# Optimization experiments

Measured on AMD Instinct MI355X. Metric: run time of the kernel, lower is better.

Reference implementation:

```python
import jax, jax.numpy as jnp
import numpy as np

N = 1024          # total nodes (includes BATCH virtual roots, processed first)
BATCH = 8         # number of trees / images
IN_DIM = 2048     # inputs_dim
EMBED = 200       # embed_dim ('start' token at row 0)
HID = 1024        # hidden_dim
NUM_CLASSES = 151 # len(classes), class 0 = background (never committed)
X_DIM = IN_DIM + EMBED


def setup_inputs() -> dict:
    key = jax.random.key(0)
    ks = jax.random.split(key, 8)
    # topologically-ordered tree: node i's parent is some j < i; first BATCH nodes are roots
    rng = np.random.RandomState(0)
    parent = np.full(N, -1, dtype=np.int64)
    for i in range(BATCH, N):
        parent[i] = rng.randint(0, i)
    sx = 1.0 / np.sqrt(X_DIM)
    sh = 1.0 / np.sqrt(HID)
    return dict(
        features=jax.random.normal(ks[0], (N, IN_DIM), jnp.float32),
        parent_idx=jnp.asarray(parent),
        batch_size=BATCH,
        W_px=jax.random.normal(ks[1], (X_DIM, HID), jnp.float32) * sx,
        b_px=jnp.zeros((HID,), jnp.float32),
        W_iofux=jax.random.normal(ks[2], (X_DIM, 5 * HID), jnp.float32) * sx,
        b_iofux=jnp.zeros((5 * HID,), jnp.float32),
        W_iofuh=jax.random.normal(ks[3], (HID, 5 * HID), jnp.float32) * sh,
        b_iofuh=jnp.zeros((5 * HID,), jnp.float32),
        W_out=jax.random.normal(ks[4], (HID, NUM_CLASSES), jnp.float32) * sh,
        b_out=jnp.zeros((NUM_CLASSES,), jnp.float32),
        embed_table=jax.random.normal(ks[5], (NUM_CLASSES + 1, EMBED), jnp.float32),
    )


def reference(features, parent_idx, batch_size, W_px, b_px, W_iofux, b_iofux,
              W_iofuh, b_iofuh, W_out, b_out, embed_table):
    n = features.shape[0]
    hid = W_iofuh.shape[0]

    def step(carry, i):
        h_all, c_all, commit_all = carry
        p = parent_idx[i]
        root = p < 0
        ps = jnp.maximum(p, 0)
        gate = jnp.where(root, 0.0, 1.0)
        ph = h_all[ps] * gate          # parent hidden (zeros at root)
        pc = c_all[ps] * gate          # parent cell   (zeros at root)
        # parent's committed label embedding; row 0 = 'start' token for roots
        pe = embed_table[jnp.where(root, 0, commit_all[ps])]
        x = jnp.concatenate([features[i], pe])          # [X_DIM]
        proj_x = x @ W_px + b_px                        # highway projection
        g = x @ W_iofux + b_iofux + ph @ W_iofuh + b_iofuh  # [5*HID]
        ig, og, fg, ug, rg = jnp.split(g, 5)
        ig = jax.nn.sigmoid(ig)
        og = jax.nn.sigmoid(og)
        fg = jax.nn.sigmoid(fg)
        rg = jax.nn.sigmoid(rg)
        ug = jnp.tanh(ug)
        c = ig * ug + fg * pc
        h = og * jnp.tanh(c)
        h_final = rg * h + (1.0 - rg) * proj_x          # highway output
        dist = h_final @ W_out + b_out                  # class logits
        # greedy commitment, background (class 0) excluded
        commit = (jnp.argmax(dist[1:]) + 1).astype(jnp.int32)
        carry = (h_all.at[i].set(h_final),
                 c_all.at[i].set(c),
                 commit_all.at[i].set(commit))
        return carry, dist

    init = (jnp.zeros((n, hid), features.dtype),
            jnp.zeros((n, hid), features.dtype),
            jnp.zeros((n,), jnp.int32))
    (h_all, c_all, commit_all), dists = jax.lax.scan(step, init, jnp.arange(n))
    # order puts the batch_size virtual roots last; they are then dropped
    out_dists = dists[batch_size:]
    out_commitments = jnp.concatenate(
        [commit_all[batch_size:], jnp.zeros((batch_size,), jnp.int32)])
    return out_dists, out_commitments
```

## Files before the change

### kernel.cpp

```cpp
#include <hip/hip_runtime.h>
#include <math.h>


#define NBLK 512
#define NTHR 512
#define OUT_COMMIT_OFF (1016 * 151)

typedef short bf16x8 __attribute__((ext_vector_type(8)));
typedef float f32x16 __attribute__((ext_vector_type(16)));

__device__ __align__(16) short g_Wih_hi[160 * 128 * 32 * 8 + 512];
__device__ __align__(16) short g_Wih_lo[160 * 128 * 32 * 8 + 512];
__device__ __align__(16) short g_Wpre_hi[192 * 256 * 32 * 8 + 512];
__device__ __align__(16) short g_Wpre_lo[192 * 256 * 32 * 8 + 512];
__device__ __align__(16) short g_fpk_hi[32 * 256 * 32 * 8 + 512];
__device__ __align__(16) short g_fpk_lo[32 * 256 * 32 * 8 + 512];
__device__ __align__(16) unsigned g_Apk_hi[128 * 128 * 32 * 4 + 256];
__device__ __align__(16) unsigned g_Apk_lo[128 * 128 * 32 * 4 + 256];
__device__ __align__(16) unsigned g_Spk_hi[128 * 128 * 32 * 4 + 256];
__device__ __align__(16) unsigned g_Spk_lo[128 * 128 * 32 * 4 + 256];
__device__ __align__(16) short g_Wout_hi[5 * 128 * 32 * 8 + 512];
__device__ __align__(16) short g_Wout_lo[5 * 128 * 32 * 8 + 512];

__device__ __align__(16) float g_c[1024 * 1024];
__device__ __align__(16) float g_pre[1024 * 6144];
__device__ __align__(16) float g_gate[1120 * 5120];
__device__ __align__(16) float g_embG[152 * 6144];
__device__ __align__(16) float g_embpad[162 * 224];
__device__ __align__(16) float g_zero[128];
__device__ __align__(16) float g_pamax_v[128 * 32 * 5 + 64];
__device__ __align__(16) int   g_pamax_i[128 * 32 * 5 + 64];
__device__ int g_lvl_start[1025];
__device__ int g_tile_off[1025];
__device__ int g_order[1024];
__device__ int g_prow[1024];
__device__ int g_cstart[1025];
__device__ int g_clist[1024];
__device__ int g_numlvl;
__device__ unsigned g_barcnt[512];

__device__ __forceinline__ unsigned short bf16_rn(float x) {
  union { float f; unsigned u; } v; v.f = x;
  unsigned r = v.u + 0x7fffu + ((v.u >> 16) & 1u);
  return (unsigned short)(r >> 16);
}
__device__ __forceinline__ float bf16_tof(unsigned short h) {
  union { float f; unsigned u; } v; v.u = ((unsigned)h) << 16; return v.f;
}
__device__ __forceinline__ void split2(float x, unsigned short& hi, unsigned short& lo) {
  hi = bf16_rn(x);
  lo = bf16_rn(x - bf16_tof(hi));
}
__device__ __forceinline__ f32x16 mfma3(bf16x8 ah, bf16x8 al, bf16x8 bh, bf16x8 bl, f32x16 c) {
  c = __builtin_amdgcn_mfma_f32_32x32x16_bf16(ah, bh, c, 0, 0, 0);
  c = __builtin_amdgcn_mfma_f32_32x32x16_bf16(ah, bl, c, 0, 0, 0);
  c = __builtin_amdgcn_mfma_f32_32x32x16_bf16(al, bh, c, 0, 0, 0);
  return c;
}

#define AST_F(p, v)  __hip_atomic_store((p), (v), __ATOMIC_RELAXED, __HIP_MEMORY_SCOPE_AGENT)
#define AST_U(p, v)  __hip_atomic_store((p), (v), __ATOMIC_RELAXED, __HIP_MEMORY_SCOPE_AGENT)

#define LD8(p, o) (*(const bf16x8*)((p) + (o)))

template<int NS>
__device__ __forceinline__ f32x16 gemm1x(const short* __restrict__ pah,
                                         const short* __restrict__ pal,
                                         const short* __restrict__ pbh,
                                         const short* __restrict__ pbl) {
  f32x16 acc = {};
  bf16x8 ahe = LD8(pah, 0),   ale = LD8(pal, 0);
  bf16x8 bhe = LD8(pbh, 0),   ble = LD8(pbl, 0);
  bf16x8 aho = LD8(pah, 512), alo = LD8(pal, 512);
  bf16x8 bho = LD8(pbh, 512), blo = LD8(pbl, 512);
  for (int g = 0; g + 1 < NS / 2; ++g) {
    const size_t o = (size_t)(2 * g + 2) * 512;
    acc = mfma3(ahe, ale, bhe, ble, acc);
    ahe = LD8(pah, o); ale = LD8(pal, o); bhe = LD8(pbh, o); ble = LD8(pbl, o);
    acc = mfma3(aho, alo, bho, blo, acc);
    aho = LD8(pah, o + 512); alo = LD8(pal, o + 512);
    bho = LD8(pbh, o + 512); blo = LD8(pbl, o + 512);
  }
  acc = mfma3(ahe, ale, bhe, ble, acc);
  acc = mfma3(aho, alo, bho, blo, acc);
  return acc;
}

template<int NS>
__device__ __forceinline__ void gemm2x(const short* __restrict__ pa0h, const short* __restrict__ pa0l,
                                       const short* __restrict__ pa1h, const short* __restrict__ pa1l,
                                       const short* __restrict__ pbh,  const short* __restrict__ pbl,
                                       f32x16& acc0, f32x16& acc1) {
  bf16x8 a0he = LD8(pa0h, 0),   a0le = LD8(pa0l, 0);
  bf16x8 a1he = LD8(pa1h, 0),   a1le = LD8(pa1l, 0);
  bf16x8 bhe  = LD8(pbh, 0),    ble  = LD8(pbl, 0);
  bf16x8 a0ho = LD8(pa0h, 512), a0lo = LD8(pa0l, 512);
  bf16x8 a1ho = LD8(pa1h, 512), a1lo = LD8(pa1l, 512);
  bf16x8 bho  = LD8(pbh, 512),  blo  = LD8(pbl, 512);
  for (int g = 0; g + 1 < NS / 2; ++g) {
    const size_t o = (size_t)(2 * g + 2) * 512;
    acc0 = mfma3(a0he, a0le, bhe, ble, acc0);
    acc1 = mfma3(a1he, a1le, bhe, ble, acc1);
    a0he = LD8(pa0h, o); a0le = LD8(pa0l, o);
    a1he = LD8(pa1h, o); a1le = LD8(pa1l, o);
    bhe = LD8(pbh, o);   ble = LD8(pbl, o);
    acc0 = mfma3(a0ho, a0lo, bho, blo, acc0);
    acc1 = mfma3(a1ho, a1lo, bho, blo, acc1);
    a0ho = LD8(pa0h, o + 512); a0lo = LD8(pa0l, o + 512);
    a1ho = LD8(pa1h, o + 512); a1lo = LD8(pa1l, o + 512);
    bho = LD8(pbh, o + 512);   blo = LD8(pbl, o + 512);
  }
  acc0 = mfma3(a0he, a0le, bhe, ble, acc0);
  acc1 = mfma3(a1he, a1le, bhe, ble, acc1);
  acc0 = mfma3(a0ho, a0lo, bho, blo, acc0);
  acc1 = mfma3(a1ho, a1lo, bho, blo, acc1);
}

__device__ __forceinline__ void gload_lds16(const float* g, float* s) {
  __builtin_amdgcn_global_load_lds(
      (const __attribute__((address_space(1))) void*)g,
      (__attribute__((address_space(3))) void*)s, 16, 0, 0);
}

__device__ __forceinline__ void gbar(unsigned int* gen) {
  __syncthreads();
  if (threadIdx.x == 0) {
    ++(*gen);
    __hip_atomic_fetch_add(&g_barcnt[((unsigned)blockIdx.x & 15) << 5], 1u,
                           __ATOMIC_RELAXED, __HIP_MEMORY_SCOPE_AGENT);
    const unsigned int target = (unsigned int)NBLK * (*gen);
    for (;;) {
      unsigned int s = 0;
      #pragma unroll
      for (int i = 0; i < 16; ++i)
        s += __hip_atomic_load(&g_barcnt[i << 5], __ATOMIC_RELAXED, __HIP_MEMORY_SCOPE_AGENT);
      if (s >= target) break;
      __builtin_amdgcn_s_sleep(8);
    }
  }
  __syncthreads();
}

__device__ __forceinline__ int pamax_combine(int prow) {
  float bv = -3.4e38f; int bi = 1;
  #pragma unroll
  for (int nt = 0; nt < 5; ++nt) {
    const float v = g_pamax_v[prow * 5 + nt];
    const int ii = g_pamax_i[prow * 5 + nt];
    if (v > bv) { bv = v; bi = ii; }
  }
  return bi;
}

__global__ void prep_kernel(const int* __restrict__ parent,
                            const float* __restrict__ emb,
                            float* __restrict__ out) {
  __shared__ int lvl[1024];
  __shared__ int cnt[1024];
  __shared__ int c2[1024];
  __shared__ int changed;
  const int i = threadIdx.x;
  const int p = parent[i];
  lvl[i] = (p < 0) ? 0 : -1;
  for (;;) {
    if (i == 0) changed = 0;
    __syncthreads();
    if (lvl[i] < 0 && lvl[p] >= 0) { lvl[i] = lvl[p] + 1; changed = 1; }
    __syncthreads();
    const int ch = changed;
    __syncthreads();
    if (ch == 0) break;
  }
  cnt[i] = 0;
  __syncthreads();
  atomicAdd(&cnt[lvl[i]], 1);
  __syncthreads();
  if (i == 0) {
    int acc = 0, nl = 0, ta = 0;
    for (int l2 = 0; l2 < 1024; ++l2) {
      g_lvl_start[l2] = acc;
      g_tile_off[l2] = ta;
      if (cnt[l2] > 0) nl = l2 + 1;
      acc += cnt[l2];
      ta += (cnt[l2] + 31) >> 5;
    }
    g_lvl_start[1024] = acc;
    g_tile_off[1024] = ta;
    g_numlvl = nl;
  }
  __syncthreads();
  cnt[i] = 0;
  __syncthreads();
  {
    const int ni = atomicAdd(&cnt[lvl[i]], 1);
    g_order[g_lvl_start[lvl[i]] + ni] = i;
    g_prow[i] = ((g_tile_off[lvl[i]] + (ni >> 5)) << 5) | (ni & 31);
  }
  __syncthreads();
  cnt[i] = 0;
  __syncthreads();
  if (p >= 0) atomicAdd(&cnt[p], 1);
  __syncthreads();
  if (i == 0) {
    int a2 = 0;
    for (int n2 = 0; n2 < 1024; ++n2) { g_cstart[n2] = a2; a2 += cnt[n2]; }
    g_cstart[1024] = a2;
  }
  __syncthreads();
  c2[i] = 0;
  __syncthreads();
  if (p >= 0) {
    const int q = g_cstart[p] + atomicAdd(&c2[p], 1);
    g_clist[q] = i;
  }
  for (int j = i; j < 162 * 224; j += 1024) {
    const int r = j / 224, cc = j - r * 224;
    g_embpad[j] = (r < 152 && cc < 200) ? emb[r * 200 + cc] : 0.0f;
  }
  __syncthreads();
  {
    const int n0 = g_tile_off[1] * 16384;
    for (int e = i; e < n0; e += 1024) { g_Apk_hi[e] = 0u; g_Apk_lo[e] = 0u; }
  }
  if (i < 512) g_barcnt[i] = 0u;
  if (i < 128) g_zero[i] = 0.0f;
  if (i < 8) out[OUT_COMMIT_OFF + 1016 + i] = 0.0f;
}

#define U_WIH  (160 * 128 * 32)
#define U_WPRE (192 * 256 * 32)
#define U_FEAT (32 * 256 * 32)
#define U_WOUT (5 * 128 * 32)
__global__ void pack_all(const float* __restrict__ Wpx, const float* __restrict__ Wix,
                         const float* __restrict__ Wih, const float* __restrict__ feat,
                         const float* __restrict__ Wout) {
  const int tot = U_WIH + U_WPRE + U_FEAT + U_WOUT;
  for (int u = blockIdx.x * blockDim.x + threadIdx.x; u < tot; u += gridDim.x * blockDim.x) {
    if (u < U_WIH) {
      const int j = u & 31, kb = (u >> 5) & 127, nt = u >> 12;
      const int n = nt * 32 + j;
      #pragma unroll
      for (int kk = 0; kk < 8; ++kk) {
        unsigned short h, l;
        split2(Wih[(size_t)(kb * 8 + kk) * 5120 + n], h, l);
        g_Wih_hi[(size_t)u * 8 + kk] = (short)h;
        g_Wih_lo[(size_t)u * 8 + kk] = (short)l;
      }
    } else if (u < U_WIH + U_WPRE) {
      const int u2 = u - U_WIH;
      const int j = u2 & 31, kb = (u2 >> 5) & 255, nt = u2 >> 13;
      const int n = nt * 32 + j;
      #pragma unroll
      for (int kk = 0; kk < 8; ++kk) {
        const int k = kb * 8 + kk;
        const float v = (n < 1024) ? Wpx[(size_t)k * 1024 + n]
                                   : Wix[(size_t)k * 5120 + (n - 1024)];
        unsigned short h, l; split2(v, h, l);
        g_Wpre_hi[(size_t)u2 * 8 + kk] = (short)h;
        g_Wpre_lo[(size_t)u2 * 8 + kk] = (short)l;
      }
    } else if (u < U_WIH + U_WPRE + U_FEAT) {
      const int u3 = u - U_WIH - U_WPRE;
      const int j = u3 & 31, kb = (u3 >> 5) & 255, mt = u3 >> 13;
      const int m = mt * 32 + j;
      #pragma unroll
      for (int kk = 0; kk < 8; ++kk) {
        unsigned short h, l;
        split2(feat[(size_t)m * 2048 + kb * 8 + kk], h, l);
        g_fpk_hi[(size_t)u3 * 8 + kk] = (short)h;
        g_fpk_lo[(size_t)u3 * 8 + kk] = (short)l;
      }
    } else {
      const int u4 = u - U_WIH - U_WPRE - U_FEAT;
      const int j = u4 & 31, kb = (u4 >> 5) & 127, nt = u4 >> 12;
      const int col = nt * 32 + j;
      #pragma unroll
      for (int kk = 0; kk < 8; ++kk) {
        const float v = (col < 151) ? Wout[(size_t)(kb * 8 + kk) * 151 + col] : 0.f;
        unsigned short h, l; split2(v, h, l);
        g_Wout_hi[(size_t)u4 * 8 + kk] = (short)h;
        g_Wout_lo[(size_t)u4 * 8 + kk] = (short)l;
      }
    }
  }
}

#define STEP(ACC, AV)                                  \
  ACC.x += AV.x * b0.x; ACC.y += AV.x * b0.y;          \
  ACC.x += AV.y * b1.x; ACC.y += AV.y * b1.y;          \
  ACC.x += AV.z * b2.x; ACC.y += AV.z * b2.y;          \
  ACC.x += AV.w * b3.x; ACC.y += AV.w * b3.y;

__device__ __forceinline__ void chunk_fma64(const float* __restrict__ Ab,
                                            const float* __restrict__ Bb,
                                            int l, float2* acc) {
  #pragma unroll
  for (int kq = 0; kq < 16; ++kq) {
    const float4 a0 = *(const float4*)(Ab + 0 * 64 + (kq << 2));
    const float4 a1 = *(const float4*)(Ab + 1 * 64 + (kq << 2));
    const float4 a2 = *(const float4*)(Ab + 2 * 64 + (kq << 2));
    const float4 a3 = *(const float4*)(Ab + 3 * 64 + (kq << 2));
    const float2 b0 = *(const float2*)(Bb + ((kq << 2) + 0) * 128 + (l << 1));
    const float2 b1 = *(const float2*)(Bb + ((kq << 2) + 1) * 128 + (l << 1));
    const float2 b2 = *(const float2*)(Bb + ((kq << 2) + 2) * 128 + (l << 1));
    const float2 b3 = *(const float2*)(Bb + ((kq << 2) + 3) * 128 + (l << 1));
    STEP(acc[0], a0) STEP(acc[1], a1) STEP(acc[2], a2) STEP(acc[3], a3)
  }
}

__global__ __launch_bounds__(512, 2) void emb_gemm(
    const float* __restrict__ Wpx, const float* __restrict__ Wix,
    const float* __restrict__ bpx, const float* __restrict__ bix,
    const float* __restrict__ bih) {
  __shared__ __align__(16) float smem[20480];
  const int tid = threadIdx.x, w = tid >> 6, l = tid & 63;
  const int mt = blockIdx.x / 48, ct = blockIdx.x % 48;
  const int c0 = ct << 7;
  const bool isproj = ct < 8;
  const float* W1 = isproj ? Wpx : Wix;
  const size_t N1 = isproj ? 1024 : 5120;
  const int c0x = isproj ? c0 : c0 - 1024;
  const int arow = (mt << 5) + (w << 2) + (l >> 4);
  const float* asrc = g_embpad + arow * 224 + ((l & 15) << 2);
  const int brow = (w << 3) + (l >> 5);
  const int bcol = (l & 31) << 2;

  auto STAGE = [&](int c, int buf) {
    float* base = smem + buf * 10240;
    const int kb = c << 6;
    gload_lds16(asrc + kb, base + (w << 8));
    #pragma unroll
    for (int j = 0; j < 4; ++j) {
      const int k = kb + brow + (j << 1);
      const float* srcB = (k < 200) ? (W1 + (size_t)(2048 + k) * N1 + c0x + bcol)
                                    : (g_zero + bcol);
      gload_lds16(srcB, base + 2048 + (((w << 3) + (j << 1)) << 7));
    }
  };

  float2 acc[4] = {{0.f,0.f},{0.f,0.f},{0.f,0.f},{0.f,0.f}};
  STAGE(0, 0);
  asm volatile("s_waitcnt vmcnt(0)" ::: "memory");
  __builtin_amdgcn_s_barrier();
  const int nch = 4;
  for (int c = 0; c < nch; ++c) {
    if (c + 1 < nch) STAGE(c + 1, (c + 1) & 1);
    const int cur = c & 1;
    chunk_fma64(smem + cur * 10240 + (w << 8), smem + cur * 10240 + 2048, l, acc);
    asm volatile("s_waitcnt vmcnt(0) lgkmcnt(0)" ::: "memory");
    __builtin_amdgcn_s_barrier();
  }
  const int cc = c0 + (l << 1);
  float2 bias;
  if (isproj) { bias.x = bpx[cc]; bias.y = bpx[cc + 1]; }
  else { bias.x = bix[cc - 1024] + bih[cc - 1024]; bias.y = bix[cc - 1023] + bih[cc - 1023]; }
  #pragma unroll
  for (int i = 0; i < 4; ++i) {
    const int r = (mt << 5) + (w << 2) + i;
    if (r < 152) {
      float2 o = { acc[i].x + bias.x, acc[i].y + bias.y };
      *(float2*)(g_embG + (size_t)r * 6144 + cc) = o;
    }
  }
}

__global__ __launch_bounds__(256, 2) void pre_gemm_mfma() {
  const int tid = threadIdx.x, w = tid >> 6, l = tid & 63;
  const int mt = blockIdx.x / 48, ct = blockIdx.x % 48;
  const int lk = l >> 5, lj = l & 31;
  const size_t abase0 = ((size_t)((2 * mt) * 256 + lk) * 32 + lj) * 8;
  const size_t abase1 = abase0 + 65536;
  const int nt = ct * 4 + w;
  const size_t bbase = ((size_t)(nt * 256 + lk) * 32 + lj) * 8;
  f32x16 acc0 = {}, acc1 = {};
  gemm2x<128>(g_fpk_hi + abase0, g_fpk_lo + abase0,
              g_fpk_hi + abase1, g_fpk_lo + abase1,
              g_Wpre_hi + bbase, g_Wpre_lo + bbase, acc0, acc1);
  const int colg = ct * 128 + w * 32 + lj;
  const int rb = mt * 64 + 4 * lk;
  #pragma unroll
  for (int reg = 0; reg < 16; ++reg) {
    const int r = rb + (reg & 3) + 8 * (reg >> 2);
    g_pre[(size_t)r * 6144 + colg] = acc0[reg];
    g_pre[(size_t)(r + 32) * 6144 + colg] = acc1[reg];
  }
}

__device__ void dist_tile(int Lp, int mt, int nt, const float* __restrict__ bout,
                          float* __restrict__ out, int tid, int w, int l,
                          int lk, int lj, float* smem, float* sdist) {
  const int s0p = g_lvl_start[Lp];
  const int Mp = g_lvl_start[Lp + 1] - s0p;
  const int tg = g_tile_off[Lp] + mt;
  const size_t ab = (size_t)tg * 32768 + (size_t)w * 4096 + (size_t)((lk << 5) + lj) * 8;
  const size_t bb = (size_t)nt * 32768 + (size_t)w * 4096 + (size_t)((lk << 5) + lj) * 8;
  f32x16 part = gemm1x<8>((const short*)g_Spk_hi + ab, (const short*)g_Spk_lo + ab,
                          g_Wout_hi + bb, g_Wout_lo + bb);
  #pragma unroll
  for (int e = 0; e < 16; ++e) smem[((e << 3) + w) * 64 + l] = part[e];
  __syncthreads();
  const int e0 = tid >> 6, lr = tid & 63;
  #pragma unroll
  for (int h = 0; h < 2; ++h) {
    const int e = e0 + (h << 3);
    float v = 0.f;
    #pragma unroll
    for (int ww = 0; ww < 8; ++ww) v += smem[((e << 3) + ww) * 64 + lr];
    const int row = (e & 3) + ((e >> 2) << 3) + ((lr >> 5) << 2);
    const int cl = lr & 31;
    const int col = (nt << 5) + cl;
    float vb = -3.4e38f;
    if (col < 151) {
      vb = v + bout[col];
      const int m = (mt << 5) + row;
      if (m < Mp) {
        const int node = g_order[s0p + m];
        if (node >= 8) out[(size_t)(node - 8) * 151 + col] = vb;
      }
    }
    sdist[row * 33 + cl] = (col >= 151 || col == 0) ? -3.4e38f : vb;
  }
  __syncthreads();
  if (tid < 32) {
    const int m = (mt << 5) + tid;
    if (m < Mp) {
      float bv = -3.4e38f; int bi = 1;
      for (int cl = 0; cl < 32; ++cl) {
        const float v = sdist[tid * 33 + cl];
        if (v > bv) { bv = v; bi = (nt << 5) + cl; }
      }
      AST_F(&g_pamax_v[(tg * 32 + tid) * 5 + nt], bv);
      AST_U(&g_pamax_i[(tg * 32 + tid) * 5 + nt], bi);
    }
  }
  __syncthreads();
}

__global__ __launch_bounds__(NTHR, 2) void lstm_main(
    const int* __restrict__ parent,
    const float* __restrict__ bout,
    float* __restrict__ out) {
  __shared__ float smem[8192];
  __shared__ float sdist[1056];
  unsigned int gen = 0;
  const int tid = threadIdx.x;
  const int bid = (int)blockIdx.x;
  const int w = tid >> 6, l = tid & 63;
  const int lk = l >> 5, lj = l & 31;
  const int nl = g_numlvl;
  const int x = bid & 7, u = bid >> 3;

  for (int L = 0; L < nl; ++L) {
    const int s0 = g_lvl_start[L];
    const int M  = g_lvl_start[L + 1] - s0;
    const int nmt = (M + 31) >> 5;
    const int toffL = g_tile_off[L];
    const int s0p = (L > 0) ? g_lvl_start[L - 1] : 0;
    const int Mp = (L > 0) ? (s0 - s0p) : 0;
    const int nmtp = (Mp + 31) >> 5;
    const int D = nmtp * 5;

    if (L > 0 && bid < D) {
      dist_tile(L - 1, bid / 5, bid % 5, bout, out, tid, w, l, lk, lj, smem, sdist);
    }
    {
      const int TPX = nmt * 20;
      for (int t = u; t < TPX; t += 64) {
        const int mt = t / 20, ci = t - (t / 20) * 20;
        const int ct = x + (ci << 3);
        const int tg = toffL + mt;
        const size_t ab = (size_t)tg * 32768 + (size_t)w * 4096 + (size_t)((lk << 5) + lj) * 8;
        const size_t bb = (size_t)ct * 32768 + (size_t)w * 4096 + (size_t)((lk << 5) + lj) * 8;
        f32x16 part = gemm1x<8>((const short*)g_Apk_hi + ab, (const short*)g_Apk_lo + ab,
                                g_Wih_hi + bb, g_Wih_lo + bb);
        #pragma unroll
        for (int e = 0; e < 16; ++e) smem[((e << 3) + w) * 64 + l] = part[e];
        __syncthreads();
        const int e0 = tid >> 6, lr = tid & 63;
        #pragma unroll
        for (int h = 0; h < 2; ++h) {
          const int e = e0 + (h << 3);
          float v = 0.f;
          #pragma unroll
          for (int ww = 0; ww < 8; ++ww) v += smem[((e << 3) + ww) * 64 + lr];
          const int row = (e & 3) + ((e >> 2) << 3) + ((lr >> 5) << 2);
          const int m = (mt << 5) + row;
          if (m < M) {
            const int col = (ct << 5) + (lr & 31);
            AST_F(&g_gate[(size_t)(s0 + m) * 5120 + col], v);
          }
        }
        __syncthreads();
      }
    }
    gbar(&gen);

    if (L > 0) {
      for (int ni2 = bid; ni2 < Mp; ni2 += NBLK) {
        const int pn = g_order[s0p + ni2];
        if (pn >= 8 && tid == 0)
          out[OUT_COMMIT_OFF + pn - 8] = (float)pamax_combine(g_prow[pn]);
      }
    }
    for (int ni = bid; ni < M; ni += NBLK) {
      const int node = g_order[s0 + ni];
      const int p = parent[node];
      const int er = (p < 0) ? 0 : pamax_combine(g_prow[p]);
      const float* gt = g_gate + (size_t)(s0 + ni) * 5120;
      const float* pre = g_pre + (size_t)node * 6144;
      const float* eg  = g_embG + (size_t)er * 6144;
      const int prow = g_prow[node];
      const size_t sbase = (size_t)(prow >> 5) * 16384 + (size_t)(prow & 31) * 4;
      const int cs = g_cstart[node], ce = g_cstart[node + 1];
      const int j = tid << 1;
      const float2 g0 = *(const float2*)(gt + j);
      const float2 g1 = *(const float2*)(gt + 1024 + j);
      const float2 g2 = *(const float2*)(gt + 2048 + j);
      const float2 g3 = *(const float2*)(gt + 3072 + j);
      const float2 g4 = *(const float2*)(gt + 4096 + j);
      const float2 p0 = *(const float2*)(pre + j);
      const float2 p1 = *(const float2*)(pre + 1024 + j);
      const float2 p2 = *(const float2*)(pre + 2048 + j);
      const float2 p3 = *(const float2*)(pre + 3072 + j);
      const float2 p4 = *(const float2*)(pre + 4096 + j);
      const float2 p5 = *(const float2*)(pre + 5120 + j);
      const float2 e0v = *(const float2*)(eg + j);
      const float2 e1 = *(const float2*)(eg + 1024 + j);
      const float2 e2 = *(const float2*)(eg + 2048 + j);
      const float2 e3 = *(const float2*)(eg + 3072 + j);
      const float2 e4 = *(const float2*)(eg + 4096 + j);
      const float2 e5 = *(const float2*)(eg + 5120 + j);
      float2 pc2 = {0.f, 0.f};
      if (p >= 0) pc2 = *(const float2*)(g_c + (size_t)p * 1024 + j);

      float cv[2], hf[2];
      #pragma unroll
      for (int e = 0; e < 2; ++e) {
        const float proj = ((e == 0) ? p0.x : p0.y) + ((e == 0) ? e0v.x : e0v.y);
        const float vi = ((e == 0) ? g0.x : g0.y) + ((e == 0) ? p1.x : p1.y) + ((e == 0) ? e1.x : e1.y);
        const float vo = ((e == 0) ? g1.x : g1.y) + ((e == 0) ? p2.x : p2.y) + ((e == 0) ? e2.x : e2.y);
        const float vf = ((e == 0) ? g2.x : g2.y) + ((e == 0) ? p3.x : p3.y) + ((e == 0) ? e3.x : e3.y);
        const float vu = ((e == 0) ? g3.x : g3.y) + ((e == 0) ? p4.x : p4.y) + ((e == 0) ? e4.x : e4.y);
        const float vr = ((e == 0) ? g4.x : g4.y) + ((e == 0) ? p5.x : p5.y) + ((e == 0) ? e5.x : e5.y);
        const float ig = 1.f / (1.f + expf(-vi));
        const float og = 1.f / (1.f + expf(-vo));
        const float fg = 1.f / (1.f + expf(-vf));
        const float rg = 1.f / (1.f + expf(-vr));
        const float ug = tanhf(vu);
        const float pc = (e == 0) ? pc2.x : pc2.y;
        const float c = ig * ug + fg * pc;
        const float h = og * tanhf(c);
        cv[e] = c;
        hf[e] = rg * h + (1.f - rg) * proj;
      }
      AST_F(&g_c[(size_t)node * 1024 + j], cv[0]);
      AST_F(&g_c[(size_t)node * 1024 + j + 1], cv[1]);
      unsigned short h0, l0, h1, l1;
      split2(hf[0], h0, l0);
      split2(hf[1], h1, l1);
      const unsigned hpk = (unsigned)h0 | ((unsigned)h1 << 16);
      const unsigned lpk = (unsigned)l0 | ((unsigned)l1 << 16);
      const size_t soff = sbase + (size_t)(j >> 3) * 128 + ((j & 7) >> 1);
      AST_U(&g_Spk_hi[soff], hpk);
      AST_U(&g_Spk_lo[soff], lpk);
      for (int ci = cs; ci < ce; ++ci) {
        const int prc = g_prow[g_clist[ci]];
        const size_t aoff = (size_t)(prc >> 5) * 16384 + (size_t)(j >> 3) * 128
                          + (size_t)(prc & 31) * 4 + ((j & 7) >> 1);
        AST_U(&g_Apk_hi[aoff], hpk);
        AST_U(&g_Apk_lo[aoff], lpk);
      }
    }
    gbar(&gen);
  }

  {
    const int Lf = nl - 1;
    const int s0f = g_lvl_start[Lf];
    const int Mf = g_lvl_start[Lf + 1] - s0f;
    const int nmtf = (Mf + 31) >> 5;
    const int Df = nmtf * 5;
    if (bid < Df) {
      dist_tile(Lf, bid / 5, bid % 5, bout, out, tid, w, l, lk, lj, smem, sdist);
    }
    gbar(&gen);
    for (int ni = bid; ni < Mf; ni += NBLK) {
      const int pn = g_order[s0f + ni];
      if (pn >= 8 && tid == 0)
        out[OUT_COMMIT_OFF + pn - 8] = (float)pamax_combine(g_prow[pn]);
    }
  }
}

extern "C" void kernel_launch(void* const* d_in, const int* in_sizes, int n_in,
                              void* d_out, int out_size, void* d_ws, size_t ws_size,
                              hipStream_t stream) {
  const float* feat   = (const float*)d_in[0];
  const int*   parent = (const int*)d_in[1];
  const float* Wpx  = (const float*)d_in[3];
  const float* bpx  = (const float*)d_in[4];
  const float* Wix  = (const float*)d_in[5];
  const float* bix  = (const float*)d_in[6];
  const float* Wih  = (const float*)d_in[7];
  const float* bih  = (const float*)d_in[8];
  const float* Wout = (const float*)d_in[9];
  const float* bout = (const float*)d_in[10];
  const float* emb  = (const float*)d_in[11];
  float* out = (float*)d_out;

  hipLaunchKernelGGL(prep_kernel, dim3(1), dim3(1024), 0, stream, parent, emb, out);
  hipLaunchKernelGGL(pack_all, dim3(2048), dim3(256), 0, stream, Wpx, Wix, Wih, feat, Wout);
  hipLaunchKernelGGL(emb_gemm, dim3(240), dim3(512), 0, stream, Wpx, Wix, bpx, bix, bih);
  hipLaunchKernelGGL(pre_gemm_mfma, dim3(768), dim3(256), 0, stream);
  hipLaunchKernelGGL(lstm_main, dim3(NBLK), dim3(NTHR), 0, stream,
                     parent, bout, out);
}
```

Baseline: 673.8 us.

## Merge pre-GEMM, embedding GEMM and Wih/Wout packing into one fill kernel

```diff
diff --git a/kernel.cpp b/kernel.cpp
--- a/kernel.cpp
+++ b/kernel.cpp
@@ -28,8 +28,7 @@
 __device__ __align__(16) float g_embG[152 * 6144];
 __device__ __align__(16) float g_embpad[162 * 224];
 __device__ __align__(16) float g_zero[128];
-__device__ __align__(16) float g_pamax_v[128 * 32 * 5 + 64];
-__device__ __align__(16) int   g_pamax_i[128 * 32 * 5 + 64];
+__device__ __align__(16) unsigned long long g_pamax[128 * 32 * 5 + 64];
 __device__ int g_lvl_start[1025];
 __device__ int g_tile_off[1025];
 __device__ int g_order[1024];
@@ -135,7 +134,7 @@
       for (int i = 0; i < 16; ++i)
         s += __hip_atomic_load(&g_barcnt[i << 5], __ATOMIC_RELAXED, __HIP_MEMORY_SCOPE_AGENT);
       if (s >= target) break;
-      __builtin_amdgcn_s_sleep(8);
+      __builtin_amdgcn_s_sleep(1);
     }
   }
   __syncthreads();
@@ -145,9 +144,9 @@
   float bv = -3.4e38f; int bi = 1;
   #pragma unroll
   for (int nt = 0; nt < 5; ++nt) {
-    const float v = g_pamax_v[prow * 5 + nt];
-    const int ii = g_pamax_i[prow * 5 + nt];
-    if (v > bv) { bv = v; bi = ii; }
+    const unsigned long long pu = g_pamax[prow * 5 + nt];
+    const float v = __uint_as_float((unsigned)pu);
+    if (v > bv) { bv = v; bi = (int)(pu >> 32); }
   }
   return bi;
 }
@@ -227,28 +226,14 @@
   if (i < 8) out[OUT_COMMIT_OFF + 1016 + i] = 0.0f;
 }
 
-#define U_WIH  (160 * 128 * 32)
 #define U_WPRE (192 * 256 * 32)
 #define U_FEAT (32 * 256 * 32)
-#define U_WOUT (5 * 128 * 32)
-__global__ void pack_all(const float* __restrict__ Wpx, const float* __restrict__ Wix,
-                         const float* __restrict__ Wih, const float* __restrict__ feat,
-                         const float* __restrict__ Wout) {
-  const int tot = U_WIH + U_WPRE + U_FEAT + U_WOUT;
+__global__ void packPF(const float* __restrict__ Wpx, const float* __restrict__ Wix,
+                       const float* __restrict__ feat) {
+  const int tot = U_WPRE + U_FEAT;
   for (int u = blockIdx.x * blockDim.x + threadIdx.x; u < tot; u += gridDim.x * blockDim.x) {
-    if (u < U_WIH) {
-      const int j = u & 31, kb = (u >> 5) & 127, nt = u >> 12;
-      const int n = nt * 32 + j;
-      #pragma unroll
-      for (int kk = 0; kk < 8; ++kk) {
-        unsigned short h, l;
-        split2(Wih[(size_t)(kb * 8 + kk) * 5120 + n], h, l);
-        g_Wih_hi[(size_t)u * 8 + kk] = (short)h;
-        g_Wih_lo[(size_t)u * 8 + kk] = (short)l;
-      }
-    } else if (u < U_WIH + U_WPRE) {
-      const int u2 = u - U_WIH;
-      const int j = u2 & 31, kb = (u2 >> 5) & 255, nt = u2 >> 13;
+    if (u < U_WPRE) {
+      const int j = u & 31, kb = (u >> 5) & 255, nt = u >> 13;
       const int n = nt * 32 + j;
       #pragma unroll
       for (int kk = 0; kk < 8; ++kk) {
@@ -256,11 +241,11 @@
         const float v = (n < 1024) ? Wpx[(size_t)k * 1024 + n]
                                    : Wix[(size_t)k * 5120 + (n - 1024)];
         unsigned short h, l; split2(v, h, l);
-        g_Wpre_hi[(size_t)u2 * 8 + kk] = (short)h;
-        g_Wpre_lo[(size_t)u2 * 8 + kk] = (short)l;
-      }
-    } else if (u < U_WIH + U_WPRE + U_FEAT) {
-      const int u3 = u - U_WIH - U_WPRE;
+        g_Wpre_hi[(size_t)u * 8 + kk] = (short)h;
+        g_Wpre_lo[(size_t)u * 8 + kk] = (short)l;
+      }
+    } else {
+      const int u3 = u - U_WPRE;
       const int j = u3 & 31, kb = (u3 >> 5) & 255, mt = u3 >> 13;
       const int m = mt * 32 + j;
       #pragma unroll
@@ -269,17 +254,6 @@
         split2(feat[(size_t)m * 2048 + kb * 8 + kk], h, l);
         g_fpk_hi[(size_t)u3 * 8 + kk] = (short)h;
         g_fpk_lo[(size_t)u3 * 8 + kk] = (short)l;
-      }
-    } else {
-      const int u4 = u - U_WIH - U_WPRE - U_FEAT;
-      const int j = u4 & 31, kb = (u4 >> 5) & 127, nt = u4 >> 12;
-      const int col = nt * 32 + j;
-      #pragma unroll
-      for (int kk = 0; kk < 8; ++kk) {
-        const float v = (col < 151) ? Wout[(size_t)(kb * 8 + kk) * 151 + col] : 0.f;
-        unsigned short h, l; split2(v, h, l);
-        g_Wout_hi[(size_t)u4 * 8 + kk] = (short)h;
-        g_Wout_lo[(size_t)u4 * 8 + kk] = (short)l;
       }
     }
   }
@@ -308,81 +282,129 @@
   }
 }
 
-__global__ __launch_bounds__(512, 2) void emb_gemm(
+#define U_WIH  (160 * 128 * 32)
+#define U_WOUT (5 * 128 * 32)
+#define NT_EMB  240
+#define NT_WIH  320
+#define NT_SOUP (NT_EMB + NT_WIH + 1)
+
+__global__ __launch_bounds__(512, 2) void fill_kernel(
     const float* __restrict__ Wpx, const float* __restrict__ Wix,
     const float* __restrict__ bpx, const float* __restrict__ bix,
-    const float* __restrict__ bih) {
+    const float* __restrict__ bih, const float* __restrict__ Wih,
+    const float* __restrict__ Wout) {
   __shared__ __align__(16) float smem[20480];
-  const int tid = threadIdx.x, w = tid >> 6, l = tid & 63;
-  const int mt = blockIdx.x / 48, ct = blockIdx.x % 48;
-  const int c0 = ct << 7;
-  const bool isproj = ct < 8;
-  const float* W1 = isproj ? Wpx : Wix;
-  const size_t N1 = isproj ? 1024 : 5120;
-  const int c0x = isproj ? c0 : c0 - 1024;
-  const int arow = (mt << 5) + (w << 2) + (l >> 4);
-  const float* asrc = g_embpad + arow * 224 + ((l & 15) << 2);
-  const int brow = (w << 3) + (l >> 5);
-  const int bcol = (l & 31) << 2;
-
-  auto STAGE = [&](int c, int buf) {
-    float* base = smem + buf * 10240;
-    const int kb = c << 6;
-    gload_lds16(asrc + kb, base + (w << 8));
-    #pragma unroll
-    for (int j = 0; j < 4; ++j) {
-      const int k = kb + brow + (j << 1);
-      const float* srcB = (k < 200) ? (W1 + (size_t)(2048 + k) * N1 + c0x + bcol)
-                                    : (g_zero + bcol);
-      gload_lds16(srcB, base + 2048 + (((w << 3) + (j << 1)) << 7));
-    }
-  };
-
-  float2 acc[4] = {{0.f,0.f},{0.f,0.f},{0.f,0.f},{0.f,0.f}};
-  STAGE(0, 0);
-  asm volatile("s_waitcnt vmcnt(0)" ::: "memory");
-  __builtin_amdgcn_s_barrier();
-  const int nch = 4;
-  for (int c = 0; c < nch; ++c) {
-    if (c + 1 < nch) STAGE(c + 1, (c + 1) & 1);
-    const int cur = c & 1;
-    chunk_fma64(smem + cur * 10240 + (w << 8), smem + cur * 10240 + 2048, l, acc);
-    asm volatile("s_waitcnt vmcnt(0) lgkmcnt(0)" ::: "memory");
-    __builtin_amdgcn_s_barrier();
-  }
-  const int cc = c0 + (l << 1);
-  float2 bias;
-  if (isproj) { bias.x = bpx[cc]; bias.y = bpx[cc + 1]; }
-  else { bias.x = bix[cc - 1024] + bih[cc - 1024]; bias.y = bix[cc - 1023] + bih[cc - 1023]; }
-  #pragma unroll
-  for (int i = 0; i < 4; ++i) {
-    const int r = (mt << 5) + (w << 2) + i;
-    if (r < 152) {
-      float2 o = { acc[i].x + bias.x, acc[i].y + bias.y };
-      *(float2*)(g_embG + (size_t)r * 6144 + cc) = o;
-    }
-  }
-}
-
-__global__ __launch_bounds__(256, 2) void pre_gemm_mfma() {
-  const int tid = threadIdx.x, w = tid >> 6, l = tid & 63;
-  const int mt = blockIdx.x / 48, ct = blockIdx.x % 48;
-  const int lk = l >> 5, lj = l & 31;
-  const size_t abase0 = ((size_t)((2 * mt) * 256 + lk) * 32 + lj) * 8;
-  const size_t abase1 = abase0 + 65536;
-  const int nt = ct * 4 + w;
-  const size_t bbase = ((size_t)(nt * 256 + lk) * 32 + lj) * 8;
-  f32x16 acc0 = {}, acc1 = {};
-  gemm2x<128>(g_fpk_hi + abase0, g_fpk_lo + abase0,
-              g_fpk_hi + abase1, g_fpk_lo + abase1,
-              g_Wpre_hi + bbase, g_Wpre_lo + bbase, acc0, acc1);
-  const int colg = ct * 128 + w * 32 + lj;
-  const int rb = mt * 64 + 4 * lk;
-  #pragma unroll
-  for (int reg = 0; reg < 16; ++reg) {
-    const int r = rb + (reg & 3) + 8 * (reg >> 2);
-    g_pre[(size_t)r * 6144 + colg] = acc0[reg];
-    g_pre[(size_t)(r + 32) * 6144 + colg] = acc1[reg];
+  const int bid = (int)blockIdx.x, tid = threadIdx.x;
+  const int l = tid & 63;
+
+  {
+    const int x = bid & 7, q = bid >> 3;
+    if (q < 48) {
+      const int sel = tid >> 8;
+      const int w4 = (tid >> 6) & 3;
+      const int lk = l >> 5, lj = l & 31;
+      const int e = 2 * q + sel;
+      const int ct = x + ((e % 6) << 3);
+      const int mt = e / 6;
+      const size_t abase0 = ((size_t)((2 * mt) * 256 + lk) * 32 + lj) * 8;
+      const size_t abase1 = abase0 + 65536;
+      const int nt = ct * 4 + w4;
+      const size_t bbase = ((size_t)(nt * 256 + lk) * 32 + lj) * 8;
+      f32x16 acc0 = {}, acc1 = {};
+      gemm2x<128>(g_fpk_hi + abase0, g_fpk_lo + abase0,
+                  g_fpk_hi + abase1, g_fpk_lo + abase1,
+                  g_Wpre_hi + bbase, g_Wpre_lo + bbase, acc0, acc1);
+      const int colg = ct * 128 + w4 * 32 + lj;
+      const int rb = mt * 64 + 4 * lk;
+      #pragma unroll
+      for (int reg = 0; reg < 16; ++reg) {
+        const int r = rb + (reg & 3) + 8 * (reg >> 2);
+        g_pre[(size_t)r * 6144 + colg] = acc0[reg];
+        g_pre[(size_t)(r + 32) * 6144 + colg] = acc1[reg];
+      }
+    }
+  }
+  __syncthreads();
+
+  for (int t = bid; t < NT_SOUP; t += 512) {
+    if (t < NT_EMB) {
+      const int w = tid >> 6;
+      const int mt = t / 48, ct = t % 48;
+      const int c0 = ct << 7;
+      const bool isproj = ct < 8;
+      const float* W1 = isproj ? Wpx : Wix;
+      const size_t N1 = isproj ? 1024 : 5120;
+      const int c0x = isproj ? c0 : c0 - 1024;
+      const int arow = (mt << 5) + (w << 2) + (l >> 4);
+      const float* asrc = g_embpad + arow * 224 + ((l & 15) << 2);
+      const int brow = (w << 3) + (l >> 5);
+      const int bcol = (l & 31) << 2;
+
+      auto STAGE = [&](int c, int buf) {
+        float* base = smem + buf * 10240;
+        const int kb = c << 6;
+        gload_lds16(asrc + kb, base + (w << 8));
+        #pragma unroll
+        for (int j = 0; j < 4; ++j) {
+          const int k = kb + brow + (j << 1);
+          const float* srcB = (k < 200) ? (W1 + (size_t)(2048 + k) * N1 + c0x + bcol)
+                                        : (g_zero + bcol);
+          gload_lds16(srcB, base + 2048 + (((w << 3) + (j << 1)) << 7));
+        }
+      };
+
+      float2 acc[4] = {{0.f,0.f},{0.f,0.f},{0.f,0.f},{0.f,0.f}};
+      STAGE(0, 0);
+      asm volatile("s_waitcnt vmcnt(0)" ::: "memory");
+      __builtin_amdgcn_s_barrier();
+      for (int c = 0; c < 4; ++c) {
+        if (c + 1 < 4) STAGE(c + 1, (c + 1) & 1);
+        const int cur = c & 1;
+        chunk_fma64(smem + cur * 10240 + (w << 8), smem + cur * 10240 + 2048, l, acc);
+        asm volatile("s_waitcnt vmcnt(0) lgkmcnt(0)" ::: "memory");
+        __builtin_amdgcn_s_barrier();
+      }
+      const int cc = c0 + (l << 1);
+      float2 bias;
+      if (isproj) { bias.x = bpx[cc]; bias.y = bpx[cc + 1]; }
+      else { bias.x = bix[cc - 1024] + bih[cc - 1024]; bias.y = bix[cc - 1023] + bih[cc - 1023]; }
+      #pragma unroll
+      for (int i = 0; i < 4; ++i) {
+        const int r = (mt << 5) + (w << 2) + i;
+        if (r < 152) {
+          float2 o = { acc[i].x + bias.x, acc[i].y + bias.y };
+          *(float2*)(g_embG + (size_t)r * 6144 + cc) = o;
+        }
+      }
+    } else if (t < NT_EMB + NT_WIH) {
+      const int base = (t - NT_EMB) * 2048 + (tid << 2);
+      #pragma unroll
+      for (int k4 = 0; k4 < 4; ++k4) {
+        const int u = base + k4;
+        const int j = u & 31, kb = (u >> 5) & 127, nt = u >> 12;
+        const int n = nt * 32 + j;
+        #pragma unroll
+        for (int kk = 0; kk < 8; ++kk) {
+          unsigned short h, lo;
+          split2(Wih[(size_t)(kb * 8 + kk) * 5120 + n], h, lo);
+          g_Wih_hi[(size_t)u * 8 + kk] = (short)h;
+          g_Wih_lo[(size_t)u * 8 + kk] = (short)lo;
+        }
+      }
+    } else {
+      for (int u = tid; u < U_WOUT; u += 512) {
+        const int j = u & 31, kb = (u >> 5) & 127, nt = u >> 12;
+        const int col = nt * 32 + j;
+        #pragma unroll
+        for (int kk = 0; kk < 8; ++kk) {
+          const float v = (col < 151) ? Wout[(size_t)(kb * 8 + kk) * 151 + col] : 0.f;
+          unsigned short h, lo; split2(v, h, lo);
+          g_Wout_hi[(size_t)u * 8 + kk] = (short)h;
+          g_Wout_lo[(size_t)u * 8 + kk] = (short)lo;
+        }
+      }
+    }
+    __syncthreads();
   }
 }
 
@@ -429,8 +451,9 @@
         const float v = sdist[tid * 33 + cl];
         if (v > bv) { bv = v; bi = (nt << 5) + cl; }
       }
-      AST_F(&g_pamax_v[(tg * 32 + tid) * 5 + nt], bv);
-      AST_U(&g_pamax_i[(tg * 32 + tid) * 5 + nt], bi);
+      const unsigned long long pu =
+          ((unsigned long long)(unsigned)bi << 32) | (unsigned long long)__float_as_uint(bv);
+      AST_U(&g_pamax[(tg * 32 + tid) * 5 + nt], pu);
     }
   }
   __syncthreads();
@@ -448,7 +471,8 @@
   const int w = tid >> 6, l = tid & 63;
   const int lk = l >> 5, lj = l & 31;
   const int nl = g_numlvl;
-  const int x = bid & 7, u = bid >> 3;
+  const int x = bid & 7;
+  const int u2 = 63 - (bid >> 3);
 
   for (int L = 0; L < nl; ++L) {
     const int s0 = g_lvl_start[L];
@@ -465,7 +489,7 @@
     }
     {
       const int TPX = nmt * 20;
-      for (int t = u; t < TPX; t += 64) {
+      for (int t = u2; t < TPX; t += 64) {
         const int mt = t / 20, ci = t - (t / 20) * 20;
         const int ct = x + (ci << 3);
         const int tg = toffL + mt;
@@ -609,9 +633,9 @@
   float* out = (float*)d_out;
 
   hipLaunchKernelGGL(prep_kernel, dim3(1), dim3(1024), 0, stream, parent, emb, out);
-  hipLaunchKernelGGL(pack_all, dim3(2048), dim3(256), 0, stream, Wpx, Wix, Wih, feat, Wout);
-  hipLaunchKernelGGL(emb_gemm, dim3(240), dim3(512), 0, stream, Wpx, Wix, bpx, bix, bih);
-  hipLaunchKernelGGL(pre_gemm_mfma, dim3(768), dim3(256), 0, stream);
+  hipLaunchKernelGGL(packPF, dim3(2048), dim3(256), 0, stream, Wpx, Wix, feat);
+  hipLaunchKernelGGL(fill_kernel, dim3(512), dim3(512), 0, stream,
+                     Wpx, Wix, bpx, bix, bih, Wih, Wout);
   hipLaunchKernelGGL(lstm_main, dim3(NBLK), dim3(NTHR), 0, stream,
                      parent, bout, out);
 }
```

New measurement: 776.7 us. 1.15x slower.
